# Performance work log

Hardware: AMD Instinct MI355X
Metric: run time of the kernel (lower is better)

Reference implementation:

```python
import jax, jax.numpy as jnp
import numpy as np

N_FEAT = 256
B, T = 8, 2048


def setup_inputs() -> dict:
    key = jax.random.key(0)
    k1, k2, k3, k4, k5, k6 = jax.random.split(key, 6)
    feat = jax.random.normal(k1, (B, T, N_FEAT), dtype=jnp.float32)
    hlens = jax.random.randint(k2, (B,), 1, T + 1, dtype=jnp.int32)
    # torch nn.Linear params: weight [out, in], bias [out]
    lim = 1.0 / np.sqrt(N_FEAT)
    Wq = jax.random.uniform(k3, (N_FEAT, N_FEAT), jnp.float32, -lim, lim)
    bq = jax.random.uniform(k4, (N_FEAT,), jnp.float32, -lim, lim)
    Wk = jax.random.uniform(k5, (N_FEAT, N_FEAT), jnp.float32, -lim, lim)
    bk = jax.random.uniform(k6, (N_FEAT,), jnp.float32, -lim, lim)
    return {"feat": feat, "hlens": hlens, "Wq": Wq, "bq": bq, "Wk": Wk, "bk": bk}


def reference(feat, hlens, Wq, bq, Wk, bk):
    # q/k projections (torch Linear: x @ W^T + b)
    q = jnp.einsum('btf,gf->btg', feat, Wq) + bq  # [B, T, F]
    k = jnp.einsum('btf,gf->btg', feat, Wk) + bk  # [B, T, F]
    sa = jnp.einsum('btf,bsf->bts', q, k)         # [B, T, T] full score matrix
    score = jnp.mean(sa, axis=-1)                 # [B, T]
    attn = jax.nn.softmax(sa, axis=-1)            # [B, T, T]
    feat_new = jnp.einsum('bts,bsf->btf', attn, feat)  # [B, T, F]
    # peaks is overwritten to all-True in the original, so hlens_new = T and
    # the per-batch gather loop is an identity copy -> feat_new unchanged.
    hlens_new = jnp.full((feat.shape[0],), feat.shape[1], dtype=jnp.int32)
    return feat_new, hlens_new, score
```

## Files before the change

### kernel.cpp

```cpp
#include <hip/hip_runtime.h>
#include <math.h>

#define B_ 8
#define T_ 2048
#define F_ 256
#define M_TOT (B_ * T_)

typedef __attribute__((ext_vector_type(8))) short short8;
typedef __attribute__((ext_vector_type(4))) float floatx4;

__device__ __forceinline__ short f2bf(float x) {
    unsigned u = __float_as_uint(x);
    u += 0x7FFF + ((u >> 16) & 1);
    return (short)(u >> 16);
}
__device__ __forceinline__ float bf2f(short s) {
    return __uint_as_float(((unsigned)(unsigned short)s) << 16);
}

__device__ __forceinline__ void cp_g2l_16(const void* g, void* l) {
    __builtin_amdgcn_global_load_lds(
        (const __attribute__((address_space(1))) void*)g,
        (__attribute__((address_space(3))) void*)l, 16, 0, 0);
}

__global__ __launch_bounds__(256) void pack_feat_all(
    const float* __restrict__ feat,
    short* __restrict__ featAh, short* __restrict__ featAl,
    short* __restrict__ stg, float* __restrict__ featpart,
    const float* __restrict__ Wq, const float* __restrict__ Wk,
    short* __restrict__ wfqh, short* __restrict__ wfql,
    short* __restrict__ wfkh)
{
    const int tid = threadIdx.x;
    const int lane = tid & 63, w = tid >> 6;
    const int quad = lane >> 4, l15 = lane & 15;

    if (blockIdx.x == 64) {
#pragma unroll
        for (int i = 0; i < 8; ++i) {
            const int idx = blockIdx.y * 32 + w * 8 + i;
            const int isk = idx >> 7, nt = (idx >> 3) & 15, fc = idx & 7;
            const float* __restrict__ W = isk ? Wk : Wq;
            const int row = nt * 16 + l15, col = fc * 32 + quad * 8;
            float v[8];
            *(float4*)&v[0] = *(const float4*)&W[(size_t)row * F_ + col];
            *(float4*)&v[4] = *(const float4*)&W[(size_t)row * F_ + col + 4];
            const size_t dst = ((size_t)(nt * 8 + fc)) * 512 + lane * 8;
            if (isk) {
                short8 h;
#pragma unroll
                for (int j = 0; j < 8; ++j) h[j] = f2bf(v[j]);
                *(short8*)&wfkh[dst] = h;
            } else {
                short8 h, l;
#pragma unroll
                for (int j = 0; j < 8; ++j) {
                    const short hh = f2bf(v[j]);
                    h[j] = hh; l[j] = f2bf(v[j] - bf2f(hh));
                }
                *(short8*)&wfqh[dst] = h;
                *(short8*)&wfql[dst] = l;
            }
        }
        return;
    }

    __shared__ float lds[32][260];
    const int kc  = blockIdx.x;
    const int b   = blockIdx.y;

#pragma unroll
    for (int i = 0; i < 8; ++i) {
        const int lin = i * 256 + tid;
        const int r = lin >> 6, c4 = (lin & 63) * 4;
        float4 v = *(const float4*)&feat[((size_t)b * T_ + kc * 32 + r) * F_ + c4];
        lds[r][c4 + 0] = v.x; lds[r][c4 + 1] = v.y;
        lds[r][c4 + 2] = v.z; lds[r][c4 + 3] = v.w;
    }
    __syncthreads();

#pragma unroll
    for (int i = 0; i < 4; ++i) {
        const int idx = w * 4 + i;
        const int r16h = idx >> 3, fc = idx & 7;
        float v[8];
        *(float4*)&v[0] = *(const float4*)&lds[r16h * 16 + l15][fc * 32 + quad * 8];
        *(float4*)&v[4] = *(const float4*)&lds[r16h * 16 + l15][fc * 32 + quad * 8 + 4];
        short8 h, l;
#pragma unroll
        for (int j = 0; j < 8; ++j) {
            const short hh = f2bf(v[j]);
            h[j] = hh; l[j] = f2bf(v[j] - bf2f(hh));
        }
        const int r16 = b * 128 + kc * 2 + r16h;
        const size_t dst = ((size_t)r16 * 8 + fc) * 512 + lane * 8;
        __builtin_nontemporal_store(h, (short8*)&featAh[dst]);
        __builtin_nontemporal_store(l, (short8*)&featAl[dst]);
    }

#pragma unroll
    for (int fi = 0; fi < 4; ++fi) {
        const int ft = w + fi * 4;
        short8 h;
#pragma unroll
        for (int j = 0; j < 8; ++j)
            h[j] = f2bf(lds[quad * 8 + j][ft * 16 + l15]);
        const size_t dst = ((size_t)(b * 64 + kc)) * 16384 + 8192 + ft * 512 + lane * 8;
        *(short8*)&stg[dst] = h;
    }

    {
        float s = 0.f;
#pragma unroll
        for (int r = 0; r < 32; ++r) s += lds[r][tid];
        featpart[((size_t)b * 64 + kc) * 256 + tid] = s;
    }
}

__global__ __launch_bounds__(512, 4) void proj_mfma(
    const short* __restrict__ featAh, const short* __restrict__ featAl,
    const short* __restrict__ wfqh, const short* __restrict__ wfql,
    const short* __restrict__ wfkh,
    const float* __restrict__ bq, const float* __restrict__ bk,
    short* __restrict__ qfh, short* __restrict__ qfl,
    short* __restrict__ stg,
    const float* __restrict__ featpart, const float* __restrict__ Wk,
    float* __restrict__ kbar_g, float* __restrict__ out_hlens)
{
    __shared__ short wbuf[2][8192];
    __shared__ float Tr[8][16][36];

    const int tid = threadIdx.x, lane = tid & 63, w = tid >> 6;
    const int quad = lane >> 4, l15 = lane & 15;
    const int x  = blockIdx.x;

    if (x >= 512) {
        float* fb = (float*)wbuf;
        const int bb = x - 512;
        if (tid < 256) {
            float s = 0.f;
#pragma unroll 8
            for (int c = 0; c < 64; ++c)
                s += featpart[((size_t)bb * 64 + c) * 256 + tid];
            fb[tid] = s * (1.0f / (float)T_);
        }
        __syncthreads();
        if (tid < 256) {
            float acc = bk[tid];
#pragma unroll 8
            for (int f = 0; f < 256; ++f)
                acc += Wk[(size_t)tid * 256 + f] * fb[f];
            kbar_g[bb * 256 + tid] = acc;
        }
        if (bb == 0 && tid < B_) out_hlens[tid] = (float)T_;
        return;
    }

    const int ng = x >> 7, rg = x & 127;
    const bool isq = ng < 2;
    const int r16 = rg * 8 + w;
    const int b = r16 >> 7, qt16 = r16 & 127;
    const int ntb = isq ? ng * 8 : (ng - 2) * 8;

    short8 ah[8], al[8];
#pragma unroll
    for (int fc = 0; fc < 8; ++fc) {
        const size_t off = ((size_t)r16 * 8 + fc) * 512 + lane * 8;
        ah[fc] = *(const short8*)&featAh[off];
        al[fc] = *(const short8*)&featAl[off];
    }

    const short* __restrict__ wsh = (isq ? wfqh : wfkh) + (size_t)ntb * 4096;
    const short* __restrict__ wsl = wfql + (size_t)ntb * 4096;
    const float* __restrict__ bias = isq ? bq : bk;

    cp_g2l_16(wsh + tid * 8, &wbuf[0][tid * 8]);
    if (isq) cp_g2l_16(wsl + tid * 8, &wbuf[0][4096 + tid * 8]);

    int cur = 0;
    for (int i = 0; i < 8; ++i, cur ^= 1) {
        __syncthreads();

        floatx4 C = (floatx4){0.f, 0.f, 0.f, 0.f};
#pragma unroll
        for (int fc = 0; fc < 8; ++fc) {
            short8 wh = *(const short8*)&wbuf[cur][fc * 512 + lane * 8];
            C = __builtin_amdgcn_mfma_f32_16x16x32_bf16(ah[fc], wh, C, 0, 0, 0);
            C = __builtin_amdgcn_mfma_f32_16x16x32_bf16(al[fc], wh, C, 0, 0, 0);
            if (isq) {
                short8 wl2 = *(const short8*)&wbuf[cur][4096 + fc * 512 + lane * 8];
                C = __builtin_amdgcn_mfma_f32_16x16x32_bf16(ah[fc], wl2, C, 0, 0, 0);
            }
        }

        if (i + 1 < 8) {
            cp_g2l_16(wsh + (size_t)(i + 1) * 4096 + tid * 8,
                      &wbuf[cur ^ 1][tid * 8]);
            if (isq) cp_g2l_16(wsl + (size_t)(i + 1) * 4096 + tid * 8,
                               &wbuf[cur ^ 1][4096 + tid * 8]);
        }

        const int nt = ntb + i;
        const float bv = bias[nt * 16 + l15];
        const int ch = (i & 1) * 16;
#pragma unroll
        for (int r = 0; r < 4; ++r)
            Tr[w][quad * 4 + r][ch + l15] = C[r] + bv;

        if (i & 1) {
            float v[8];
            *(float4*)&v[0] = *(const float4*)&Tr[w][l15][quad * 8];
            *(float4*)&v[4] = *(const float4*)&Tr[w][l15][quad * 8 + 4];
            const int p = nt >> 1;
            if (isq) {
                short8 h, l;
#pragma unroll
                for (int j = 0; j < 8; ++j) {
                    const short hh = f2bf(v[j]);
                    h[j] = hh; l[j] = f2bf(v[j] - bf2f(hh));
                }
                const size_t dst = ((size_t)(b * 8 + p) * 128 + qt16) * 512 + lane * 8;
                __builtin_nontemporal_store(h, (short8*)&qfh[dst]);
                __builtin_nontemporal_store(l, (short8*)&qfl[dst]);
            } else {
                short8 h;
#pragma unroll
                for (int j = 0; j < 8; ++j) h[j] = f2bf(v[j]);
                const size_t dst = ((size_t)(b * 64 + (qt16 >> 1))) * 16384
                                 + (p * 2 + (qt16 & 1)) * 512 + lane * 8;
                *(short8*)&stg[dst] = h;
            }
        }
    }
}

__global__ __launch_bounds__(256, 2) void attn_mfma(
    const short* __restrict__ qfh_g, const short* __restrict__ qfl_g,
    const short* __restrict__ stg,
    float* __restrict__ o0, float* __restrict__ o1,
    float* __restrict__ lpart,
    const float* __restrict__ kbar_g, float* __restrict__ out_score)
{
    __shared__ short kbuf[2][16384];
    __shared__ float P_lds[64 * 36];
    __shared__ float l_lds[2][64];

    const int tid  = threadIdx.x;
    const int wave = tid >> 6, lane = tid & 63;
    const int qp   = wave & 1, fh = wave >> 1;
    const int quad = lane >> 4, l15 = lane & 15;

    const int lid  = blockIdx.x;
    const int b    = lid & 7;
    const int qt   = (lid >> 3) & 31;
    const int ks   = lid >> 8;

    short8 qh[2][8], ql[2][8];
#pragma unroll
    for (int t = 0; t < 2; ++t) {
        const int qt16 = qt * 4 + qp * 2 + t;
#pragma unroll
        for (int fc = 0; fc < 8; ++fc) {
            const size_t off = ((size_t)(b * 8 + fc) * 128 + qt16) * 512 + lane * 8;
            qh[t][fc] = *(const short8*)&qfh_g[off];
            ql[t][fc] = *(const short8*)&qfl_g[off];
        }
    }

    floatx4 O[2][8];
#pragma unroll
    for (int t = 0; t < 2; ++t)
#pragma unroll
        for (int i = 0; i < 8; ++i) O[t][i] = (floatx4){0.f, 0.f, 0.f, 0.f};
    float lsum[2][4] = {};

    const short* sbase = &stg[(size_t)b * 64 * 16384];
    const int kbeg = ks * 32, kend = kbeg + 32;

    {
        const short* src = sbase + (size_t)kbeg * 16384 + tid * 8;
        short* dst = &kbuf[0][tid * 8];
#pragma unroll
        for (int i = 0; i < 8; ++i)
            cp_g2l_16(src + i * 2048, dst + i * 2048);
    }

    int cur = 0;
    for (int kt = kbeg; kt < kend; ++kt, cur ^= 1) {
        __syncthreads();

        floatx4 Sa[2], Sb[2];
#pragma unroll
        for (int t = 0; t < 2; ++t) {
            Sa[t] = (floatx4){0.f, 0.f, 0.f, 0.f};
            Sb[t] = (floatx4){0.f, 0.f, 0.f, 0.f};
        }
#pragma unroll
        for (int fc = 0; fc < 8; ++fc) {
            short8 bh = *(const short8*)&kbuf[cur][(fc * 2 + fh) * 512 + lane * 8];
#pragma unroll
            for (int t = 0; t < 2; ++t) {
                Sa[t] = __builtin_amdgcn_mfma_f32_16x16x32_bf16(qh[t][fc], bh, Sa[t], 0, 0, 0);
                Sb[t] = __builtin_amdgcn_mfma_f32_16x16x32_bf16(ql[t][fc], bh, Sb[t], 0, 0, 0);
            }
        }

#pragma unroll
        for (int t = 0; t < 2; ++t)
#pragma unroll
            for (int r = 0; r < 4; ++r) {
                const float e = __expf(Sa[t][r] + Sb[t][r]);
                lsum[t][r] += e;
                P_lds[((qp * 2 + t) * 16 + quad * 4 + r) * 36 + fh * 16 + l15] = e;
            }
        __syncthreads();

        short8 ph[2];
#pragma unroll
        for (int t = 0; t < 2; ++t) {
            float pv[8];
            *(float4*)&pv[0] = *(const float4*)&P_lds[((qp * 2 + t) * 16 + l15) * 36 + quad * 8];
            *(float4*)&pv[4] = *(const float4*)&P_lds[((qp * 2 + t) * 16 + l15) * 36 + quad * 8 + 4];
#pragma unroll
            for (int j = 0; j < 8; ++j)
                ph[t][j] = f2bf(pv[j]);
        }

        if (kt + 1 < kend) {
            const short* src = sbase + (size_t)(kt + 1) * 16384 + tid * 8;
            short* dst = &kbuf[cur ^ 1][tid * 8];
#pragma unroll
            for (int i = 0; i < 8; ++i)
                cp_g2l_16(src + i * 2048, dst + i * 2048);
        }

#pragma unroll
        for (int ft = 0; ft < 8; ++ft) {
            short8 fv = *(const short8*)&kbuf[cur][8192 + (fh * 8 + ft) * 512 + lane * 8];
#pragma unroll
            for (int t = 0; t < 2; ++t)
                O[t][ft] = __builtin_amdgcn_mfma_f32_16x16x32_bf16(ph[t], fv, O[t][ft], 0, 0, 0);
        }
    }

    if (ks == 0) {
        const float* __restrict__ kb = &kbar_g[b * 256];
        float sc[2] = {0.f, 0.f};
#pragma unroll
        for (int fc = 0; fc < 8; ++fc) {
            float4 k0 = *(const float4*)&kb[fc * 32 + quad * 8];
            float4 k1 = *(const float4*)&kb[fc * 32 + quad * 8 + 4];
#pragma unroll
            for (int t = 0; t < 2; ++t) {
#pragma unroll
                for (int j = 0; j < 4; ++j) {
                    sc[t] += (bf2f(qh[t][fc][j]) + bf2f(ql[t][fc][j]))
                           * ((const float*)&k0)[j];
                    sc[t] += (bf2f(qh[t][fc][j + 4]) + bf2f(ql[t][fc][j + 4]))
                           * ((const float*)&k1)[j];
                }
            }
        }
#pragma unroll
        for (int t = 0; t < 2; ++t) {
            sc[t] += __shfl_xor(sc[t], 16, 64);
            sc[t] += __shfl_xor(sc[t], 32, 64);
            if (quad == 0)
                out_score[(size_t)b * T_ + qt * 64 + (qp * 2 + t) * 16 + l15] = sc[t];
        }
    }

#pragma unroll
    for (int t = 0; t < 2; ++t)
#pragma unroll
        for (int r = 0; r < 4; ++r) {
            lsum[t][r] += __shfl_xor(lsum[t][r], 1, 64);
            lsum[t][r] += __shfl_xor(lsum[t][r], 2, 64);
            lsum[t][r] += __shfl_xor(lsum[t][r], 4, 64);
            lsum[t][r] += __shfl_xor(lsum[t][r], 8, 64);
        }
    if (l15 == 0) {
#pragma unroll
        for (int t = 0; t < 2; ++t)
#pragma unroll
            for (int r = 0; r < 4; ++r)
                l_lds[fh][(qp * 2 + t) * 16 + quad * 4 + r] = lsum[t][r];
    }
    __syncthreads();

    float* __restrict__ opart = ks ? o1 : o0;
    const size_t row0 = (size_t)b * T_ + qt * 64;

    if (tid < 64)
        __builtin_nontemporal_store(l_lds[0][tid] + l_lds[1][tid],
                                    &lpart[(size_t)ks * M_TOT + row0 + tid]);

#pragma unroll
    for (int t = 0; t < 2; ++t)
#pragma unroll
        for (int r = 0; r < 4; ++r) {
            const int qr = (qp * 2 + t) * 16 + quad * 4 + r;
#pragma unroll
            for (int ft = 0; ft < 8; ++ft)
                __builtin_nontemporal_store(
                    O[t][ft][r],
                    &opart[(row0 + qr) * F_ + fh * 128 + ft * 16 + l15]);
        }
}

__global__ __launch_bounds__(256) void combine_kernel(
    float* __restrict__ out_feat, const float* __restrict__ o1,
    const float* __restrict__ lpart)
{
    const size_t gid = (size_t)blockIdx.x * 256 + threadIdx.x;
    const size_t row = gid >> 6;
    const float inv = 1.0f / (lpart[row] + lpart[M_TOT + row]);
    floatx4 a  = __builtin_nontemporal_load(&((const floatx4*)out_feat)[gid]);
    floatx4 bx = __builtin_nontemporal_load(&((const floatx4*)o1)[gid]);
    a = (a + bx) * inv;
    __builtin_nontemporal_store(a, &((floatx4*)out_feat)[gid]);
}

extern "C" void kernel_launch(void* const* d_in, const int* in_sizes, int n_in,
                              void* d_out, int out_size, void* d_ws, size_t ws_size,
                              hipStream_t stream)
{
    const float* feat = (const float*)d_in[0];
    const float* Wq = (const float*)d_in[2];
    const float* bq = (const float*)d_in[3];
    const float* Wk = (const float*)d_in[4];
    const float* bk = (const float*)d_in[5];

    float* out_feat  = (float*)d_out;
    float* out_hlens = out_feat + (size_t)M_TOT * F_;
    float* out_score = out_hlens + B_;

    short* featAh = (short*)d_ws;
    short* featAl = featAh + (size_t)M_TOT * F_;
    short* qfh    = featAl + (size_t)M_TOT * F_;
    short* qfl    = qfh + (size_t)M_TOT * F_;
    short* stg    = qfl + (size_t)M_TOT * F_;
    short* wfqh   = stg + (size_t)2 * M_TOT * F_;
    short* wfql   = wfqh + 65536;
    short* wfkh   = wfql + 65536;
    float* featpart = (float*)(wfkh + 65536);
    float* kbar   = featpart + 131072;
    float* o1     = (float*)featAh;
    float* lpart  = featpart;

    dim3 fgrid(65, B_);
    pack_feat_all<<<fgrid, 256, 0, stream>>>(feat, featAh, featAl, stg, featpart,
                                             Wq, Wk, wfqh, wfql, wfkh);

    proj_mfma<<<520, 512, 0, stream>>>(featAh, featAl, wfqh, wfql, wfkh,
                                       bq, bk, qfh, qfl, stg,
                                       featpart, Wk, kbar, out_hlens);

    attn_mfma<<<512, 256, 0, stream>>>(qfh, qfl, stg, out_feat, o1, lpart,
                                       kbar, out_score);

    combine_kernel<<<M_TOT * F_ / 4 / 256, 256, 0, stream>>>(out_feat, o1, lpart);
}
```

Baseline: 174.2 us.

## Fuse bf16 hi/lo split of feat into projection kernel, drop featAh/featAl buffers

The pack kernel no longer writes split bf16 hi/lo copies of feat to global memory. Instead, the projection kernel stages fp32 feat rows through LDS and converts them to hi/lo fragments in registers. The goal is to remove 16 MB of global write plus read traffic. In exchange, each projection block re-reads fp32 feat (4 blocks share the same rows), adds more syncthreads, and grows LDS via a union, which lowers the launch-bounds occupancy hint from 4 to 2.

```diff
diff --git a/kernel.cpp b/kernel.cpp
--- a/kernel.cpp
+++ b/kernel.cpp
@@ -26,7 +26,6 @@
 
 __global__ __launch_bounds__(256) void pack_feat_all(
     const float* __restrict__ feat,
-    short* __restrict__ featAh, short* __restrict__ featAl,
     short* __restrict__ stg, float* __restrict__ featpart,
     const float* __restrict__ Wq, const float* __restrict__ Wk,
     short* __restrict__ wfqh, short* __restrict__ wfql,
@@ -81,25 +80,6 @@
     __syncthreads();
 
 #pragma unroll
-    for (int i = 0; i < 4; ++i) {
-        const int idx = w * 4 + i;
-        const int r16h = idx >> 3, fc = idx & 7;
-        float v[8];
-        *(float4*)&v[0] = *(const float4*)&lds[r16h * 16 + l15][fc * 32 + quad * 8];
-        *(float4*)&v[4] = *(const float4*)&lds[r16h * 16 + l15][fc * 32 + quad * 8 + 4];
-        short8 h, l;
-#pragma unroll
-        for (int j = 0; j < 8; ++j) {
-            const short hh = f2bf(v[j]);
-            h[j] = hh; l[j] = f2bf(v[j] - bf2f(hh));
-        }
-        const int r16 = b * 128 + kc * 2 + r16h;
-        const size_t dst = ((size_t)r16 * 8 + fc) * 512 + lane * 8;
-        __builtin_nontemporal_store(h, (short8*)&featAh[dst]);
-        __builtin_nontemporal_store(l, (short8*)&featAl[dst]);
-    }
-
-#pragma unroll
     for (int fi = 0; fi < 4; ++fi) {
         const int ft = w + fi * 4;
         short8 h;
@@ -118,8 +98,15 @@
     }
 }
 
-__global__ __launch_bounds__(512, 4) void proj_mfma(
-    const short* __restrict__ featAh, const short* __restrict__ featAl,
+struct ProjLDS {
+    union {
+        float fch[32][260];
+        struct { short wbuf[2][8192]; float Tr[8][16][36]; } m;
+    } u;
+};
+
+__global__ __launch_bounds__(512, 2) void proj_mfma(
+    const float* __restrict__ feat,
     const short* __restrict__ wfqh, const short* __restrict__ wfql,
     const short* __restrict__ wfkh,
     const float* __restrict__ bq, const float* __restrict__ bk,
@@ -128,15 +115,14 @@
     const float* __restrict__ featpart, const float* __restrict__ Wk,
     float* __restrict__ kbar_g, float* __restrict__ out_hlens)
 {
-    __shared__ short wbuf[2][8192];
-    __shared__ float Tr[8][16][36];
+    __shared__ ProjLDS L;
 
     const int tid = threadIdx.x, lane = tid & 63, w = tid >> 6;
     const int quad = lane >> 4, l15 = lane & 15;
     const int x  = blockIdx.x;
 
     if (x >= 512) {
-        float* fb = (float*)wbuf;
+        float* fb = (float*)L.u.m.wbuf;
         const int bb = x - 512;
         if (tid < 256) {
             float s = 0.f;
@@ -164,19 +150,42 @@
     const int ntb = isq ? ng * 8 : (ng - 2) * 8;
 
     short8 ah[8], al[8];
-#pragma unroll
-    for (int fc = 0; fc < 8; ++fc) {
-        const size_t off = ((size_t)r16 * 8 + fc) * 512 + lane * 8;
-        ah[fc] = *(const short8*)&featAh[off];
-        al[fc] = *(const short8*)&featAl[off];
-    }
+    const size_t rowbase = (size_t)b * T_ + (rg & 15) * 128;
+#pragma unroll
+    for (int c = 0; c < 4; ++c) {
+        __syncthreads();
+#pragma unroll
+        for (int i = 0; i < 4; ++i) {
+            const int lin = i * 512 + tid;
+            const int r = lin >> 6, c4 = (lin & 63) * 4;
+            float4 v = *(const float4*)&feat[(rowbase + c * 32 + r) * F_ + c4];
+            L.u.fch[r][c4 + 0] = v.x; L.u.fch[r][c4 + 1] = v.y;
+            L.u.fch[r][c4 + 2] = v.z; L.u.fch[r][c4 + 3] = v.w;
+        }
+        __syncthreads();
+        if ((w >> 1) == c) {
+            const int h = w & 1;
+#pragma unroll
+            for (int fc = 0; fc < 8; ++fc) {
+                float v[8];
+                *(float4*)&v[0] = *(const float4*)&L.u.fch[h * 16 + l15][fc * 32 + quad * 8];
+                *(float4*)&v[4] = *(const float4*)&L.u.fch[h * 16 + l15][fc * 32 + quad * 8 + 4];
+#pragma unroll
+                for (int j = 0; j < 8; ++j) {
+                    const short hh = f2bf(v[j]);
+                    ah[fc][j] = hh; al[fc][j] = f2bf(v[j] - bf2f(hh));
+                }
+            }
+        }
+    }
+    __syncthreads();
 
     const short* __restrict__ wsh = (isq ? wfqh : wfkh) + (size_t)ntb * 4096;
     const short* __restrict__ wsl = wfql + (size_t)ntb * 4096;
     const float* __restrict__ bias = isq ? bq : bk;
 
-    cp_g2l_16(wsh + tid * 8, &wbuf[0][tid * 8]);
-    if (isq) cp_g2l_16(wsl + tid * 8, &wbuf[0][4096 + tid * 8]);
+    cp_g2l_16(wsh + tid * 8, &L.u.m.wbuf[0][tid * 8]);
+    if (isq) cp_g2l_16(wsl + tid * 8, &L.u.m.wbuf[0][4096 + tid * 8]);
 
     int cur = 0;
     for (int i = 0; i < 8; ++i, cur ^= 1) {
@@ -185,20 +194,20 @@
         floatx4 C = (floatx4){0.f, 0.f, 0.f, 0.f};
 #pragma unroll
         for (int fc = 0; fc < 8; ++fc) {
-            short8 wh = *(const short8*)&wbuf[cur][fc * 512 + lane * 8];
+            short8 wh = *(const short8*)&L.u.m.wbuf[cur][fc * 512 + lane * 8];
             C = __builtin_amdgcn_mfma_f32_16x16x32_bf16(ah[fc], wh, C, 0, 0, 0);
             C = __builtin_amdgcn_mfma_f32_16x16x32_bf16(al[fc], wh, C, 0, 0, 0);
             if (isq) {
-                short8 wl2 = *(const short8*)&wbuf[cur][4096 + fc * 512 + lane * 8];
+                short8 wl2 = *(const short8*)&L.u.m.wbuf[cur][4096 + fc * 512 + lane * 8];
                 C = __builtin_amdgcn_mfma_f32_16x16x32_bf16(ah[fc], wl2, C, 0, 0, 0);
             }
         }
 
         if (i + 1 < 8) {
             cp_g2l_16(wsh + (size_t)(i + 1) * 4096 + tid * 8,
-                      &wbuf[cur ^ 1][tid * 8]);
+                      &L.u.m.wbuf[cur ^ 1][tid * 8]);
             if (isq) cp_g2l_16(wsl + (size_t)(i + 1) * 4096 + tid * 8,
-                               &wbuf[cur ^ 1][4096 + tid * 8]);
+                               &L.u.m.wbuf[cur ^ 1][4096 + tid * 8]);
         }
 
         const int nt = ntb + i;
@@ -206,12 +215,12 @@
         const int ch = (i & 1) * 16;
 #pragma unroll
         for (int r = 0; r < 4; ++r)
-            Tr[w][quad * 4 + r][ch + l15] = C[r] + bv;
+            L.u.m.Tr[w][quad * 4 + r][ch + l15] = C[r] + bv;
 
         if (i & 1) {
             float v[8];
-            *(float4*)&v[0] = *(const float4*)&Tr[w][l15][quad * 8];
-            *(float4*)&v[4] = *(const float4*)&Tr[w][l15][quad * 8 + 4];
+            *(float4*)&v[0] = *(const float4*)&L.u.m.Tr[w][l15][quad * 8];
+            *(float4*)&v[4] = *(const float4*)&L.u.m.Tr[w][l15][quad * 8 + 4];
             const int p = nt >> 1;
             if (isq) {
                 short8 h, l;
@@ -436,9 +445,7 @@
     float* out_hlens = out_feat + (size_t)M_TOT * F_;
     float* out_score = out_hlens + B_;
 
-    short* featAh = (short*)d_ws;
-    short* featAl = featAh + (size_t)M_TOT * F_;
-    short* qfh    = featAl + (size_t)M_TOT * F_;
+    short* qfh    = (short*)d_ws;
     short* qfl    = qfh + (size_t)M_TOT * F_;
     short* stg    = qfl + (size_t)M_TOT * F_;
     short* wfqh   = stg + (size_t)2 * M_TOT * F_;
@@ -446,14 +453,14 @@
     short* wfkh   = wfql + 65536;
     float* featpart = (float*)(wfkh + 65536);
     float* kbar   = featpart + 131072;
-    float* o1     = (float*)featAh;
+    float* o1     = kbar + 2048;
     float* lpart  = featpart;
 
     dim3 fgrid(65, B_);
-    pack_feat_all<<<fgrid, 256, 0, stream>>>(feat, featAh, featAl, stg, featpart,
+    pack_feat_all<<<fgrid, 256, 0, stream>>>(feat, stg, featpart,
                                              Wq, Wk, wfqh, wfql, wfkh);
 
-    proj_mfma<<<520, 512, 0, stream>>>(featAh, featAl, wfqh, wfql, wfkh,
+    proj_mfma<<<520, 512, 0, stream>>>(feat, wfqh, wfql, wfkh,
                                        bq, bk, qfh, qfl, stg,
                                        featpart, Wk, kbar, out_hlens);
 
```

Result: slower. 193.8 us (+11.3%).
